# Optimization experiments

Measured on AMD Instinct MI355X. Metric: run time of the kernel, lower is better.

The kernel has to match this reference:

```python
import jax, jax.numpy as jnp
import numpy as np

# --- dims (match init_kwargs) ---
VOCAB = 16; D_MODEL = 512; NLAYERS = 4; LMAX = 1024; NCLASSES = 2
D_STATE = 128; D_CONV = 4; EXPAND = 2; HEADDIM = 64; PAD_IDX = 4
D_INNER = EXPAND * D_MODEL            # 1024
NHEADS = D_INNER // HEADDIM           # 16
CONV_DIM = D_INNER + 2 * D_STATE      # 1280 (ngroups=1)
D_IN_PROJ = 2 * D_INNER + 2 * D_STATE + NHEADS  # 2320
BATCH = 8; SEQ = 1024
EPS = 1e-5


def silu(x):
    return x * jax.nn.sigmoid(x)


def setup_inputs() -> dict:
    key = jax.random.key(0)
    ks = jax.random.split(key, 24)
    s = 0.02
    emb = jax.random.normal(ks[0], (VOCAB, D_MODEL), jnp.float32) * s
    emb = emb.at[PAD_IDX].set(0.0)  # padding_idx row is zero
    inp = {
        "tokens": jax.random.randint(ks[1], (BATCH, SEQ), 0, VOCAB),
        "attention_mask": jnp.ones((BATCH, SEQ), jnp.float32),
        "emb": emb,
        "pos_emb": jax.random.normal(ks[2], (1, LMAX, D_MODEL), jnp.float32) * s,
        "inp_w": jax.random.normal(ks[3], (D_MODEL, D_MODEL), jnp.float32) * s,
        "inp_b": jnp.zeros((D_MODEL,), jnp.float32),
        "ln_g": jnp.ones((D_MODEL,), jnp.float32),
        "ln_b": jnp.zeros((D_MODEL,), jnp.float32),
        # stacked per-layer Mamba2 params
        "in_proj_w": jax.random.normal(ks[4], (NLAYERS, D_IN_PROJ, D_MODEL), jnp.float32) * s,
        "conv_w": jax.random.normal(ks[5], (NLAYERS, CONV_DIM, D_CONV), jnp.float32) * 0.2,
        "conv_b": jnp.zeros((NLAYERS, CONV_DIM), jnp.float32),
        "dt_bias": jax.random.uniform(ks[6], (NLAYERS, NHEADS), jnp.float32, -4.0, -1.0),
        "A_log": jnp.log(jax.random.uniform(ks[7], (NLAYERS, NHEADS), jnp.float32, 1.0, 16.0)),
        "Dparam": jnp.ones((NLAYERS, NHEADS), jnp.float32),
        "norm_w": jnp.ones((NLAYERS, D_INNER), jnp.float32),
        "out_proj_w": jax.random.normal(ks[8], (NLAYERS, D_MODEL, D_INNER), jnp.float32) * s,
        "pooler_w": jax.random.normal(ks[9], (D_MODEL, D_MODEL), jnp.float32) * s,
        "pooler_b": jnp.zeros((D_MODEL,), jnp.float32),
        "cls_w1": jax.random.normal(ks[10], (D_MODEL // 2, D_MODEL), jnp.float32) * s,
        "cls_b1": jnp.zeros((D_MODEL // 2,), jnp.float32),
        "cls_w2": jax.random.normal(ks[11], (NCLASSES, D_MODEL // 2), jnp.float32) * s,
        "cls_b2": jnp.zeros((NCLASSES,), jnp.float32),
    }
    return inp


def mamba2_block(x, in_proj_w, conv_w, conv_b, dt_bias, A_log, Dp, norm_w, out_proj_w):
    """Mamba2 (ngroups=1, no proj biases, conv bias) on x:(B,L,d_model)."""
    Bsz, L, _ = x.shape
    zxbcdt = jnp.einsum("bld,ed->ble", x, in_proj_w)  # (B,L,2320)
    z = zxbcdt[..., :D_INNER]
    xBC = zxbcdt[..., D_INNER:D_INNER + CONV_DIM]
    dt = zxbcdt[..., D_INNER + CONV_DIM:]             # (B,L,H)
    # causal depthwise conv1d + silu
    xp = jnp.pad(xBC, ((0, 0), (D_CONV - 1, 0), (0, 0)))
    conv = conv_b
    for k in range(D_CONV):
        conv = conv + xp[:, k:k + L, :] * conv_w[:, k]
    xBC = silu(conv)
    xh = xBC[..., :D_INNER].reshape(Bsz, L, NHEADS, HEADDIM)
    Bc = xBC[..., D_INNER:D_INNER + D_STATE]          # (B,L,N)
    Cc = xBC[..., D_INNER + D_STATE:]                 # (B,L,N)
    dt = jax.nn.softplus(dt + dt_bias)                # (B,L,H)
    A = -jnp.exp(A_log)                               # (H,)
    dA = jnp.exp(dt * A)                              # (B,L,H)

    def step(h, inp):
        x_t, B_t, C_t, dt_t, dA_t = inp  # (B,H,P),(B,N),(B,N),(B,H),(B,H)
        h = h * dA_t[:, :, None, None] + (dt_t[:, :, None] * x_t)[..., None] * B_t[:, None, None, :]
        y = jnp.einsum("bhpn,bn->bhp", h, C_t)
        return h, y

    h0 = jnp.zeros((Bsz, NHEADS, HEADDIM, D_STATE), x.dtype)
    xs = (xh.transpose(1, 0, 2, 3), Bc.transpose(1, 0, 2), Cc.transpose(1, 0, 2),
          dt.transpose(1, 0, 2), dA.transpose(1, 0, 2))
    _, ys = jax.lax.scan(step, h0, xs)                # (L,B,H,P)
    y = ys.transpose(1, 0, 2, 3) + Dp[None, None, :, None] * xh
    y = y.reshape(Bsz, L, D_INNER)
    # gated RMSNorm: rmsnorm(y * silu(z)) * weight
    y = y * silu(z)
    y = y * jax.lax.rsqrt(jnp.mean(y * y, axis=-1, keepdims=True) + EPS) * norm_w
    return jnp.einsum("ble,de->bld", y, out_proj_w)


def reference(tokens, attention_mask, emb, pos_emb, inp_w, inp_b, ln_g, ln_b,
              in_proj_w, conv_w, conv_b, dt_bias, A_log, Dparam, norm_w, out_proj_w,
              pooler_w, pooler_b, cls_w1, cls_b1, cls_w2, cls_b2):
    L = tokens.shape[1]
    x = emb[tokens] + pos_emb[:, :L, :]
    # input_block: Linear -> LayerNorm (dropout is identity at eval)
    x = jnp.einsum("bld,ed->ble", x, inp_w) + inp_b
    mu = jnp.mean(x, -1, keepdims=True)
    var = jnp.mean((x - mu) ** 2, -1, keepdims=True)
    x = (x - mu) * jax.lax.rsqrt(var + EPS) * ln_g + ln_b
    x = x * attention_mask[..., None]
    for i in range(NLAYERS):
        res = x
        x = mamba2_block(x, in_proj_w[i], conv_w[i], conv_b[i], dt_bias[i],
                         A_log[i], Dparam[i], norm_w[i], out_proj_w[i])
        x = res + x
        x = x * attention_mask[..., None]
    pooled = (jnp.mean(x, axis=1) + jnp.max(x, axis=1)) * 0.5
    pooled = jax.nn.gelu(jnp.einsum("bd,ed->be", pooled, pooler_w) + pooler_b)
    h = jax.nn.gelu(jnp.einsum("bd,ed->be", pooled, cls_w1) + cls_b1)
    return jnp.einsum("bd,ed->be", h, cls_w2) + cls_b2
```

## Files before the change

### kernel.cpp

```cpp
#include <hip/hip_runtime.h>

#define EPS 1e-5f
typedef unsigned short u16;
typedef short s16x8 __attribute__((ext_vector_type(8)));
typedef float f32x4 __attribute__((ext_vector_type(4)));

__device__ __forceinline__ float siluf(float x) { return x / (1.0f + __expf(-x)); }
__device__ __forceinline__ float geluf(float x) {
    float u = 0.7978845608028654f * (x + 0.044715f * x * x * x);
    return 0.5f * x * (1.0f + tanhf(u));
}
__device__ __forceinline__ u16 f2bf(float f) {
    unsigned u = __float_as_uint(f);
    return (u16)((u + 0x7fffu + ((u >> 16) & 1u)) >> 16);
}
__device__ __forceinline__ float bf2f(u16 v) {
    return __uint_as_float(((unsigned)v) << 16);
}
struct u16x4 { u16 x, y, z, w; };
__device__ __forceinline__ u16x4 f2bf4(float4 v) {
    u16x4 r; r.x = f2bf(v.x); r.y = f2bf(v.y); r.z = f2bf(v.z); r.w = f2bf(v.w);
    return r;
}

#define GLOAD_LDS16(gp, lp) __builtin_amdgcn_global_load_lds( \
    (const __attribute__((address_space(1))) void*)(gp),      \
    (__attribute__((address_space(3))) void*)(lp), 16, 0, 0)

__global__ void k_casts(const float* __restrict__ ip, const float* __restrict__ op,
                        const float* __restrict__ inp, u16* __restrict__ wip,
                        u16* __restrict__ wop, u16* __restrict__ winp) {
    int idx = blockIdx.x * 256 + threadIdx.x;
    if (idx < 1245184) {
        int e4 = idx * 4;
        int layer = e4 / 1245184;
        int rem   = e4 - layer * 1245184;
        int row   = rem >> 9;
        int k     = rem & 511;
        float4 v = make_float4(0.f, 0.f, 0.f, 0.f);
        if (row < 2320)
            v = *(const float4*)(ip + (size_t)layer * 1187840 + (size_t)row * 512 + k);
        *(u16x4*)(wip + e4) = f2bf4(v);
    } else if (idx < 1245184 + 524288) {
        int j = idx - 1245184;
        float4 v = *(const float4*)(op + (size_t)j * 4);
        *(u16x4*)(wop + (size_t)j * 4) = f2bf4(v);
    } else if (idx < 1245184 + 524288 + 65536) {
        int j = idx - 1245184 - 524288;
        float4 v = *(const float4*)(inp + (size_t)j * 4);
        *(u16x4*)(winp + (size_t)j * 4) = f2bf4(v);
    }
}

__global__ void k_embed(const int* __restrict__ tok, const float* __restrict__ emb,
                        const float* __restrict__ pos, u16* __restrict__ out) {
    int idx = blockIdx.x * 256 + threadIdx.x;
    int d4 = idx & 127;
    int bl = idx >> 7;
    int l  = bl & 1023;
    float4 e = *(const float4*)(emb + tok[bl] * 512 + d4 * 4);
    float4 p = *(const float4*)(pos + l * 512 + d4 * 4);
    float4 v = make_float4(e.x + p.x, e.y + p.y, e.z + p.z, e.w + p.w);
    *(u16x4*)(out + (size_t)idx * 4) = f2bf4(v);
}

#define STAGE_I(buf, k0) do {                                                   \
    _Pragma("unroll")                                                           \
    for (int s_ = 0; s_ < 2; s_++) {                                            \
        int g_ = w * 2 + s_;                                                    \
        GLOAD_LDS16(A + (size_t)(m0 + g_ * 16 + lr) * 512 + (k0) + lk,          \
                    &Asm[buf][g_ * 512]);                                       \
    }                                                                           \
    GLOAD_LDS16(B + (size_t)(n0 + w * 16 + lr) * 512 + (k0) + lk,               \
                &Bsm[buf][w * 512]);                                            \
    } while (0)

#define COMPUTE_I(buf) do {                                                     \
    s16x8 af_[4], bf_[4];                                                       \
    _Pragma("unroll")                                                           \
    for (int i_ = 0; i_ < 4; i_++) {                                            \
        af_[i_] = *(const s16x8*)&Asm[buf][(wr * 4 + i_) * 512 + l * 8];        \
        bf_[i_] = *(const s16x8*)&Bsm[buf][(wc * 4 + i_) * 512 + l * 8];        \
    }                                                                           \
    _Pragma("unroll")                                                           \
    for (int i_ = 0; i_ < 4; i_++)                                              \
        _Pragma("unroll")                                                       \
        for (int j_ = 0; j_ < 4; j_++)                                          \
            acc[i_][j_] = __builtin_amdgcn_mfma_f32_16x16x32_bf16(              \
                af_[i_], bf_[j_], acc[i_][j_], 0, 0, 0);                        \
    } while (0)

__global__ __launch_bounds__(512, 4) void k_gemm_in(
    const u16* __restrict__ A, const u16* __restrict__ B,
    u16* __restrict__ zbf, u16* __restrict__ xbcbf, float* __restrict__ dtw) {
    __shared__ u16 Asm[3][8192];
    __shared__ u16 Bsm[3][4096];
    const int t = threadIdx.x;
    const int w = t >> 6, l = t & 63;
    const int wr = w >> 1, wc = w & 1;
    const int lr = l & 15, lk = (l >> 4) * 8;
    const int wgid = (blockIdx.x & 7) * 76 + (blockIdx.x >> 3);
    const int m0 = (wgid / 19) * 256;
    const int n0 = (wgid % 19) * 128;

    f32x4 acc[4][4] = {};

    STAGE_I(0, 0);
    STAGE_I(1, 32);
    for (int ki = 0; ki < 14; ki++) {
        asm volatile("s_waitcnt vmcnt(3)" ::: "memory");
        __builtin_amdgcn_s_barrier();
        STAGE_I((ki + 2) % 3, (ki + 2) * 32);
        COMPUTE_I(ki % 3);
    }
    asm volatile("s_waitcnt vmcnt(3)" ::: "memory");
    __builtin_amdgcn_s_barrier();
    COMPUTE_I(14 % 3);
    asm volatile("s_waitcnt vmcnt(0)" ::: "memory");
    __builtin_amdgcn_s_barrier();
    COMPUTE_I(15 % 3);

#pragma unroll
    for (int i = 0; i < 4; i++) {
        int mb = m0 + wr * 64 + i * 16 + (l >> 4) * 4;
#pragma unroll
        for (int j = 0; j < 4; j++) {
            int n = n0 + wc * 64 + j * 16 + (l & 15);
#pragma unroll
            for (int r2 = 0; r2 < 4; r2++) {
                int m = mb + r2;
                float v = acc[i][j][r2];
                if (n < 1024)      zbf[(size_t)m * 1024 + n] = f2bf(v);
                else if (n < 2304) xbcbf[(size_t)m * 1280 + (n - 1024)] = f2bf(v);
                else if (n < 2320) dtw[(size_t)m * 16 + (n - 2304)] = v;
            }
        }
    }
}

#define STAGE(buf, k0) do {                                                     \
    GLOAD_LDS16(A + (size_t)(m0 + w * 16 + lr) * K + (k0) + lk,                 \
                &Asm[buf][w * 512]);                                            \
    GLOAD_LDS16(B + (size_t)(n0 + w * 16 + lr) * K + (k0) + lk,                 \
                &Bsm[buf][w * 512]);                                            \
    } while (0)

#define COMPUTE(buf) do {                                                       \
    s16x8 af_[4], bf_[2];                                                       \
    _Pragma("unroll")                                                           \
    for (int i_ = 0; i_ < 4; i_++)                                              \
        af_[i_] = *(const s16x8*)&Asm[buf][(wr * 4 + i_) * 512 + l * 8];        \
    _Pragma("unroll")                                                           \
    for (int j_ = 0; j_ < 2; j_++)                                              \
        bf_[j_] = *(const s16x8*)&Bsm[buf][(wc * 2 + j_) * 512 + l * 8];        \
    _Pragma("unroll")                                                           \
    for (int i_ = 0; i_ < 4; i_++)                                              \
        _Pragma("unroll")                                                       \
        for (int j_ = 0; j_ < 2; j_++)                                          \
            acc[i_][j_] = __builtin_amdgcn_mfma_f32_16x16x32_bf16(              \
                af_[i_], bf_[j_], acc[i_][j_], 0, 0, 0);                        \
    } while (0)

template <int MODE>
__global__ __launch_bounds__(512) void k_gemm_mfma(
    const u16* __restrict__ A, const u16* __restrict__ B,
    const float* __restrict__ bias, float* __restrict__ C,
    u16* __restrict__ Cbf, const float* __restrict__ mask,
    int M, int N, int K, int gx) {
    __shared__ u16 Asm[3][4096];
    __shared__ u16 Bsm[3][4096];
    const int t = threadIdx.x;
    const int w = t >> 6, l = t & 63;
    const int wr = w >> 2, wc = w & 3;
    const int lr = l & 15, lk = (l >> 4) * 8;
    const int nwg = gridDim.x;
    const int q = nwg >> 3, r = nwg & 7;
    const int x8 = blockIdx.x & 7, d8 = blockIdx.x >> 3;
    const int wgid = (x8 < r) ? x8 * (q + 1) + d8 : r * (q + 1) + (x8 - r) * q + d8;
    const int m0 = (wgid / gx) * 128;
    const int n0 = (wgid % gx) * 128;

    f32x4 acc[4][2] = {};

    const int nk = K >> 5;
    STAGE(0, 0);
    STAGE(1, 32);
    for (int ki = 0; ki < nk - 2; ki++) {
        asm volatile("s_waitcnt vmcnt(2)" ::: "memory");
        __builtin_amdgcn_s_barrier();
        STAGE((ki + 2) % 3, (ki + 2) * 32);
        COMPUTE(ki % 3);
    }
    asm volatile("s_waitcnt vmcnt(2)" ::: "memory");
    __builtin_amdgcn_s_barrier();
    COMPUTE((nk - 2) % 3);
    asm volatile("s_waitcnt vmcnt(0)" ::: "memory");
    __builtin_amdgcn_s_barrier();
    COMPUTE((nk - 1) % 3);

#pragma unroll
    for (int i = 0; i < 4; i++) {
        int mb = m0 + wr * 64 + i * 16 + (l >> 4) * 4;
#pragma unroll
        for (int j = 0; j < 2; j++) {
            int n = n0 + wc * 32 + j * 16 + (l & 15);
#pragma unroll
            for (int r2 = 0; r2 < 4; r2++) {
                int m = mb + r2;
                float v = acc[i][j][r2];
                if (n < N) {
                    if (MODE == 1) v += bias[n];
                    size_t o = (size_t)m * N + n;
                    if (MODE == 2) {
                        v = (C[o] + v) * mask[m];
                        Cbf[o] = f2bf(v);
                    }
                    C[o] = v;
                }
            }
        }
    }
}

__global__ __launch_bounds__(128) void k_layernorm(
    float* __restrict__ x, const float* __restrict__ g,
    const float* __restrict__ b, const float* __restrict__ mask,
    u16* __restrict__ xbf) {
    __shared__ float2 sbuf[2];
    int bl = blockIdx.x;
    int t  = threadIdx.x;
    float4 v = *(float4*)(x + (size_t)bl * 512 + t * 4);
    float s = v.x + v.y + v.z + v.w;
    float q = v.x * v.x + v.y * v.y + v.z * v.z + v.w * v.w;
    for (int off = 32; off; off >>= 1) {
        s += __shfl_xor(s, off, 64);
        q += __shfl_xor(q, off, 64);
    }
    int wid = t >> 6, lane = t & 63;
    if (lane == 0) sbuf[wid] = make_float2(s, q);
    __syncthreads();
    float ts = sbuf[0].x + sbuf[1].x;
    float tq = sbuf[0].y + sbuf[1].y;
    float mu  = ts * (1.f / 512.f);
    float var = tq * (1.f / 512.f) - mu * mu;
    float inv = 1.0f / sqrtf(var + EPS);
    float mk  = mask[bl];
    float4 gg = *(const float4*)(g + t * 4);
    float4 bb = *(const float4*)(b + t * 4);
    float4 o;
    o.x = ((v.x - mu) * inv * gg.x + bb.x) * mk;
    o.y = ((v.y - mu) * inv * gg.y + bb.y) * mk;
    o.z = ((v.z - mu) * inv * gg.z + bb.z) * mk;
    o.w = ((v.w - mu) * inv * gg.w + bb.w) * mk;
    *(float4*)(x + (size_t)bl * 512 + t * 4) = o;
    *(u16x4*)(xbf + (size_t)bl * 512 + t * 4) = f2bf4(o);
}

__global__ __launch_bounds__(320) void k_conv(
    const u16* __restrict__ xbc_in, const float* __restrict__ cw,
    const float* __restrict__ cb, u16* __restrict__ xhbf,
    u16* __restrict__ bcbf) {
    int bid = blockIdx.x;
    int bl = (bid & 7) * 1024 + (bid >> 3);
    int l  = bl & 1023;
    int c  = threadIdx.x * 4;
    float4 w0 = *(const float4*)(cw + (c + 0) * 4);
    float4 w1 = *(const float4*)(cw + (c + 1) * 4);
    float4 w2 = *(const float4*)(cw + (c + 2) * 4);
    float4 w3 = *(const float4*)(cw + (c + 3) * 4);
    float4 a  = *(const float4*)(cb + c);
#pragma unroll
    for (int k = 0; k < 4; k++) {
        if (l + k - 3 >= 0) {
            u16x4 v = *(const u16x4*)(xbc_in + (size_t)(bl + k - 3) * 1280 + c);
            const float* wk0 = (const float*)&w0;
            const float* wk1 = (const float*)&w1;
            const float* wk2 = (const float*)&w2;
            const float* wk3 = (const float*)&w3;
            a.x = fmaf(bf2f(v.x), wk0[k], a.x);
            a.y = fmaf(bf2f(v.y), wk1[k], a.y);
            a.z = fmaf(bf2f(v.z), wk2[k], a.z);
            a.w = fmaf(bf2f(v.w), wk3[k], a.w);
        }
    }
    float4 o = make_float4(siluf(a.x), siluf(a.y), siluf(a.z), siluf(a.w));
    if (c < 1024)
        *(u16x4*)(xhbf + (size_t)bl * 1024 + c) = f2bf4(o);
    else
        *(u16x4*)(bcbf + (size_t)bl * 256 + (c - 1024)) = f2bf4(o);
}

__global__ __launch_bounds__(256) void k_ssd(
    const u16* __restrict__ xhbf, const u16* __restrict__ bcbf,
    const float* __restrict__ dt_raw, const float* __restrict__ dtbias,
    const float* __restrict__ alog, float* __restrict__ elbuf,
    u16* __restrict__ y16, u16* __restrict__ scb16) {
    int bid = blockIdx.x;
    int bhc = (bid & 7) * 128 + (bid >> 3);
    int c = bhc & 7, h = (bhc >> 3) & 15, b = bhc >> 7;
    const size_t row0 = (size_t)b * 1024 + c * 128;
    const int t = threadIdx.x, w = t >> 6, l = t & 63;
    const int wr = w >> 1, wc = w & 1;
    const int lr = l & 15, lk8 = (l >> 4) * 8;

    __shared__ float cl[128], dtl[128], wv[128];
    __shared__ float csh;
    __shared__ __align__(16) u16 shA[8704];
    __shared__ __align__(16) u16 shB[17408];

    float A = -__expf(alog[h]);
    float v = 0.f;
    if (t < 128) {
        float raw = dt_raw[(row0 + t) * 16 + h] + dtbias[h];
        float s = (raw > 20.f) ? raw : log1pf(__expf(raw));
        dtl[t] = s;
        v = s * A;
        int lane = t & 63;
#pragma unroll
        for (int off = 1; off < 64; off <<= 1) {
            float o = __shfl_up(v, off, 64);
            if (lane >= off) v += o;
        }
        if (t == 63) csh = v;
    }
    __syncthreads();
    if (t >= 64 && t < 128) v += csh;
    if (t < 128) {
        cl[t] = v;
        elbuf[(size_t)bhc * 128 + t] = __expf(v);
    }
    __syncthreads();
    if (t < 128) wv[t] = __expf(cl[127] - cl[t]);

    f32x4 acc[4][4] = {};
    for (int ks = 0; ks < 4; ks++) {
        int k0 = ks * 32;
#pragma unroll
        for (int s = 0; s < 2; s++) {
            int g = w * 2 + s;
            GLOAD_LDS16(bcbf + (row0 + g * 16 + lr) * 256 + 128 + k0 + lk8, &shA[g * 512]);
            GLOAD_LDS16(bcbf + (row0 + g * 16 + lr) * 256 +       k0 + lk8, &shA[4096 + g * 512]);
        }
        __syncthreads();
        s16x8 af[4], bfr[4];
#pragma unroll
        for (int i = 0; i < 4; i++) {
            af[i]  = *(const s16x8*)&shA[(wr * 4 + i) * 512 + l * 8];
            bfr[i] = *(const s16x8*)&shA[4096 + (wc * 4 + i) * 512 + l * 8];
        }
#pragma unroll
        for (int i = 0; i < 4; i++)
#pragma unroll
            for (int j = 0; j < 4; j++)
                acc[i][j] = __builtin_amdgcn_mfma_f32_16x16x32_bf16(af[i], bfr[j], acc[i][j], 0, 0, 0);
        __syncthreads();
    }

#pragma unroll
    for (int jj = 0; jj < 32; jj++) {
        int j = jj * 4 + w;
        float xv = bf2f(xhbf[(row0 + j) * 1024 + h * 64 + l]);
        shA[l * 136 + j] = f2bf(dtl[j] * xv);
    }
    __syncthreads();

    f32x4 acc2[4][2] = {};
    for (int half = 0; half < 2; half++) {
        if (wc == half) {
#pragma unroll
            for (int i = 0; i < 4; i++) {
#pragma unroll
                for (int j = 0; j < 4; j++) {
                    int col = half * 64 + j * 16 + (l & 15);
#pragma unroll
                    for (int r = 0; r < 4; r++) {
                        int row = wr * 64 + i * 16 + (l >> 4) * 4 + r;
                        float e = __expf(fminf(cl[row] - cl[col], 0.f));
                        float pv = (col <= row) ? acc[i][j][r] * e : 0.f;
                        shB[row * 72 + j * 16 + (l & 15)] = f2bf(pv);
                    }
                }
            }
        }
        __syncthreads();
#pragma unroll
        for (int ks = 0; ks < 2; ks++) {
            int kof = ks * 32;
            s16x8 pa[4], ub[2];
#pragma unroll
            for (int i = 0; i < 4; i++)
                pa[i] = *(const s16x8*)&shB[(wr * 64 + i * 16 + lr) * 72 + kof + lk8];
#pragma unroll
            for (int jj = 0; jj < 2; jj++)
                ub[jj] = *(const s16x8*)&shA[(wc * 32 + jj * 16 + lr) * 136 + half * 64 + kof + lk8];
#pragma unroll
            for (int i = 0; i < 4; i++)
#pragma unroll
                for (int jj = 0; jj < 2; jj++)
                    acc2[i][jj] = __builtin_amdgcn_mfma_f32_16x16x32_bf16(pa[i], ub[jj], acc2[i][jj], 0, 0, 0);
        }
        __syncthreads();
    }
#pragma unroll
    for (int i = 0; i < 4; i++)
#pragma unroll
        for (int jj = 0; jj < 2; jj++) {
            int p = wc * 32 + jj * 16 + (l & 15);
#pragma unroll
            for (int r = 0; r < 4; r++) {
                int row = wr * 64 + i * 16 + (l >> 4) * 4 + r;
                y16[(row0 + row) * 1024 + h * 64 + p] = f2bf(acc2[i][jj][r]);
            }
        }

#pragma unroll
    for (int s = 0; s < 64; s++) {
        int j = s * 2 + (w & 1);
        int n = (w >> 1) * 64 + l;
        float bvv = bf2f(bcbf[(row0 + j) * 256 + n]);
        shB[n * 136 + j] = f2bf(wv[j] * bvv);
    }
    __syncthreads();

    f32x4 acc3[4][2] = {};
#pragma unroll
    for (int ks = 0; ks < 4; ks++) {
        int kof = ks * 32;
        s16x8 ua[4], bb[2];
#pragma unroll
        for (int i = 0; i < 4; i++)
            ua[i] = *(const s16x8*)&shA[(i * 16 + lr) * 136 + kof + lk8];
#pragma unroll
        for (int jj = 0; jj < 2; jj++)
            bb[jj] = *(const s16x8*)&shB[(w * 32 + jj * 16 + lr) * 136 + kof + lk8];
#pragma unroll
        for (int i = 0; i < 4; i++)
#pragma unroll
            for (int jj = 0; jj < 2; jj++)
                acc3[i][jj] = __builtin_amdgcn_mfma_f32_16x16x32_bf16(ua[i], bb[jj], acc3[i][jj], 0, 0, 0);
    }
#pragma unroll
    for (int i = 0; i < 4; i++)
#pragma unroll
        for (int jj = 0; jj < 2; jj++) {
            int n = w * 32 + jj * 16 + (l & 15);
#pragma unroll
            for (int r = 0; r < 4; r++) {
                int p = i * 16 + (l >> 4) * 4 + r;
                scb16[(size_t)bhc * 8192 + (size_t)p * 128 + n] = f2bf(acc3[i][jj][r]);
            }
        }
}

__global__ __launch_bounds__(512) void k_states(u16* __restrict__ scb16,
                                                const float* __restrict__ elbuf) {
    int bh = blockIdx.x;
    int t = threadIdx.x;
    float hreg[16];
#pragma unroll
    for (int j = 0; j < 16; j++) hreg[j] = 0.f;
    size_t o = (size_t)t * 16;
    for (int c = 0; c < 8; c++) {
        int bhc = bh * 8 + c;
        float Tc = elbuf[(size_t)bhc * 128 + 127];
        u16* p = scb16 + (size_t)bhc * 8192 + o;
        s16x8 v0 = *(s16x8*)(p);
        s16x8 v1 = *(s16x8*)(p + 8);
        s16x8 o0, o1;
#pragma unroll
        for (int j = 0; j < 8; j++) {
            o0[j] = (short)f2bf(hreg[j]);
            o1[j] = (short)f2bf(hreg[8 + j]);
        }
        *(s16x8*)(p)     = o0;
        *(s16x8*)(p + 8) = o1;
#pragma unroll
        for (int j = 0; j < 8; j++) {
            hreg[j]     = fmaf(Tc, hreg[j],     bf2f((u16)v0[j]));
            hreg[8 + j] = fmaf(Tc, hreg[8 + j], bf2f((u16)v1[j]));
        }
    }
}

__global__ __launch_bounds__(256) void k_inter(
    const u16* __restrict__ xhbf, const u16* __restrict__ bcbf,
    const float* __restrict__ elbuf, const u16* __restrict__ scb16,
    const float* __restrict__ Dp, u16* __restrict__ y16) {
    int bid = blockIdx.x;
    int bhc = (bid & 7) * 128 + (bid >> 3);
    int c = bhc & 7, h = (bhc >> 3) & 15, b = bhc >> 7;
    const size_t row0 = (size_t)b * 1024 + c * 128;
    const int t = threadIdx.x, w = t >> 6, l = t & 63;
    const int wr = w >> 1, wc = w & 1;
    const int lr = l & 15, lk8 = (l >> 4) * 8;
    __shared__ __align__(16) u16 CStg[4096];
    __shared__ __align__(16) u16 HStg[2048];
    __shared__ float el[128];
    if (t < 128) el[t] = elbuf[(size_t)bhc * 128 + t];
    float Dv = Dp[h];

    f32x4 acc[4][2] = {};
    for (int ks = 0; ks < 4; ks++) {
        int k0 = ks * 32;
#pragma unroll
        for (int s = 0; s < 2; s++) {
            int g = w * 2 + s;
            GLOAD_LDS16(bcbf + (row0 + g * 16 + lr) * 256 + 128 + k0 + lk8, &CStg[g * 512]);
        }
        GLOAD_LDS16(scb16 + (size_t)bhc * 8192 + (size_t)(w * 16 + lr) * 128 + k0 + lk8,
                    &HStg[w * 512]);
        __syncthreads();
        s16x8 ca[4], hb[2];
#pragma unroll
        for (int i = 0; i < 4; i++)
            ca[i] = *(const s16x8*)&CStg[(wr * 4 + i) * 512 + l * 8];
#pragma unroll
        for (int jj = 0; jj < 2; jj++)
            hb[jj] = *(const s16x8*)&HStg[(wc * 2 + jj) * 512 + l * 8];
#pragma unroll
        for (int i = 0; i < 4; i++)
#pragma unroll
            for (int jj = 0; jj < 2; jj++)
                acc[i][jj] = __builtin_amdgcn_mfma_f32_16x16x32_bf16(ca[i], hb[jj], acc[i][jj], 0, 0, 0);
        __syncthreads();
    }
#pragma unroll
    for (int i = 0; i < 4; i++)
#pragma unroll
        for (int jj = 0; jj < 2; jj++) {
            int p = wc * 32 + jj * 16 + (l & 15);
#pragma unroll
            for (int r = 0; r < 4; r++) {
                int lrow = wr * 64 + i * 16 + (l >> 4) * 4 + r;
                size_t yo = (row0 + lrow) * 1024 + h * 64 + p;
                float yv = bf2f(y16[yo]) + el[lrow] * acc[i][jj][r]
                         + Dv * bf2f(xhbf[(row0 + lrow) * 1024 + h * 64 + p]);
                y16[yo] = f2bf(yv);
            }
        }
}

__global__ __launch_bounds__(256) void k_gate(
    const u16* __restrict__ y16, const u16* __restrict__ zbf,
    const float* __restrict__ nw, u16* __restrict__ ybf) {
    __shared__ float sbuf[4];
    int bl = blockIdx.x;
    int t  = threadIdx.x;
    u16x4 yv4 = *(const u16x4*)(y16 + (size_t)bl * 1024 + t * 4);
    u16x4 zv4 = *(const u16x4*)(zbf + (size_t)bl * 1024 + t * 4);
    float4 gv;
    gv.x = bf2f(yv4.x) * siluf(bf2f(zv4.x));
    gv.y = bf2f(yv4.y) * siluf(bf2f(zv4.y));
    gv.z = bf2f(yv4.z) * siluf(bf2f(zv4.z));
    gv.w = bf2f(yv4.w) * siluf(bf2f(zv4.w));
    float q = gv.x * gv.x + gv.y * gv.y + gv.z * gv.z + gv.w * gv.w;
    for (int off = 32; off; off >>= 1) q += __shfl_xor(q, off, 64);
    int wid = t >> 6, lane = t & 63;
    if (lane == 0) sbuf[wid] = q;
    __syncthreads();
    float tot = sbuf[0] + sbuf[1] + sbuf[2] + sbuf[3];
    float scale = 1.0f / sqrtf(tot * (1.f / 1024.f) + EPS);
    float4 nv = *(const float4*)(nw + t * 4);
    float4 o;
    o.x = gv.x * scale * nv.x;
    o.y = gv.y * scale * nv.y;
    o.z = gv.z * scale * nv.z;
    o.w = gv.w * scale * nv.w;
    *(u16x4*)(ybf + (size_t)bl * 1024 + t * 4) = f2bf4(o);
}

__global__ __launch_bounds__(256) void k_pool1(const float* __restrict__ x,
                                               float* __restrict__ psum,
                                               float* __restrict__ pmax) {
    int blk = blockIdx.x;
    int b = blk >> 6, lc = blk & 63;
    int t = threadIdx.x;
    const float* px = x + (size_t)b * 524288 + (size_t)lc * 16 * 512;
    float s0 = 0.f, s1 = 0.f, m0 = -3.0e38f, m1 = -3.0e38f;
#pragma unroll
    for (int r = 0; r < 16; r++) {
        float v0 = px[r * 512 + t];
        float v1 = px[r * 512 + t + 256];
        s0 += v0; s1 += v1;
        m0 = fmaxf(m0, v0); m1 = fmaxf(m1, v1);
    }
    psum[(size_t)blk * 512 + t]       = s0;
    psum[(size_t)blk * 512 + t + 256] = s1;
    pmax[(size_t)blk * 512 + t]       = m0;
    pmax[(size_t)blk * 512 + t + 256] = m1;
}

__global__ __launch_bounds__(256) void k_pool2(const float* __restrict__ psum,
                                               const float* __restrict__ pmax,
                                               float* __restrict__ pooled) {
    int idx = blockIdx.x * 256 + threadIdx.x;
    int b = idx >> 9, d = idx & 511;
    float s = 0.f, m = -3.0e38f;
    for (int c = 0; c < 64; c++) {
        s += psum[((size_t)b * 64 + c) * 512 + d];
        m = fmaxf(m, pmax[((size_t)b * 64 + c) * 512 + d]);
    }
    pooled[idx] = 0.5f * (s * (1.f / 1024.f) + m);
}

template <int ACT>
__global__ void k_fc(const float* __restrict__ in, const float* __restrict__ W,
                     const float* __restrict__ bias, float* __restrict__ out,
                     int BN, int N, int K) {
    int idx = blockIdx.x * 64 + threadIdx.x;
    if (idx >= BN) return;
    int b = idx / N, n = idx % N;
    const float* a = in + (size_t)b * K;
    const float* w = W + (size_t)n * K;
    float acc = 0.f;
    for (int k = 0; k < K; k += 4) {
        float4 av = *(const float4*)(a + k);
        float4 wv = *(const float4*)(w + k);
        acc += av.x * wv.x + av.y * wv.y + av.z * wv.z + av.w * wv.w;
    }
    float v = acc + bias[n];
    if (ACT == 1) v = geluf(v);
    out[idx] = v;
}

extern "C" void kernel_launch(void* const* d_in, const int* in_sizes, int n_in,
                              void* d_out, int out_size, void* d_ws, size_t ws_size,
                              hipStream_t stream) {
    (void)in_sizes; (void)n_in; (void)out_size; (void)ws_size;
    const int*   tok        = (const int*)  d_in[0];
    const float* mask       = (const float*)d_in[1];
    const float* emb        = (const float*)d_in[2];
    const float* pos        = (const float*)d_in[3];
    const float* inp_w      = (const float*)d_in[4];
    const float* inp_b      = (const float*)d_in[5];
    const float* ln_g       = (const float*)d_in[6];
    const float* ln_b       = (const float*)d_in[7];
    const float* in_proj_w  = (const float*)d_in[8];
    const float* conv_w     = (const float*)d_in[9];
    const float* conv_b     = (const float*)d_in[10];
    const float* dt_bias    = (const float*)d_in[11];
    const float* A_log      = (const float*)d_in[12];
    const float* Dparam     = (const float*)d_in[13];
    const float* norm_w     = (const float*)d_in[14];
    const float* out_proj_w = (const float*)d_in[15];
    const float* pooler_w   = (const float*)d_in[16];
    const float* pooler_b   = (const float*)d_in[17];
    const float* cls_w1     = (const float*)d_in[18];
    const float* cls_b1     = (const float*)d_in[19];
    const float* cls_w2     = (const float*)d_in[20];
    const float* cls_b2     = (const float*)d_in[21];
    float* out = (float*)d_out;

    float* ws     = (float*)d_ws;
    float* x      = ws;
    float* dt_raw = x + (size_t)8192 * 512;
    float* elbuf  = dt_raw + (size_t)8192 * 16;
    float* psum   = elbuf + 131072;
    float* pmax   = psum + 262144;
    float* pooled = pmax + 262144;
    float* pbuf   = pooled + 4096;
    float* cbuf   = pbuf + 4096;
    u16* x_bf    = (u16*)(cbuf + 2048);
    u16* z_bf    = x_bf + (size_t)8192 * 512;
    u16* xbc_in  = z_bf + (size_t)8192 * 1024;
    u16* y_bf    = xbc_in + (size_t)8192 * 1280;
    u16* xhbf    = y_bf + (size_t)8192 * 1024;
    u16* bcbf    = xhbf + (size_t)8192 * 1024;
    u16* y16     = bcbf + (size_t)8192 * 256;
    u16* wip_bf  = y16 + (size_t)8192 * 1024;
    u16* wop_bf  = wip_bf + (size_t)4 * 2432 * 512;
    u16* winp_bf = wop_bf + (size_t)4 * 512 * 1024;
    u16* xe_bf   = (u16*)y16;
    u16* scb16   = xbc_in;

    k_casts<<<7168, 256, 0, stream>>>(in_proj_w, out_proj_w, inp_w,
                                      wip_bf, wop_bf, winp_bf);

    k_embed<<<4096, 256, 0, stream>>>(tok, emb, pos, xe_bf);
    k_gemm_mfma<1><<<256, 512, 0, stream>>>(xe_bf, winp_bf, inp_b, x, nullptr,
                                            nullptr, 8192, 512, 512, 4);
    k_layernorm<<<8192, 128, 0, stream>>>(x, ln_g, ln_b, mask, x_bf);

    for (int i = 0; i < 4; i++) {
        k_gemm_in<<<608, 512, 0, stream>>>(x_bf, wip_bf + (size_t)i * 2432 * 512,
                                           z_bf, xbc_in, dt_raw);
        k_conv<<<8192, 320, 0, stream>>>(xbc_in, conv_w + (size_t)i * 1280 * 4,
                                         conv_b + (size_t)i * 1280, xhbf, bcbf);
        k_ssd<<<1024, 256, 0, stream>>>(xhbf, bcbf, dt_raw, dt_bias + i * 16,
                                        A_log + i * 16, elbuf, y16, scb16);
        k_states<<<128, 512, 0, stream>>>(scb16, elbuf);
        k_inter<<<1024, 256, 0, stream>>>(xhbf, bcbf, elbuf, scb16,
                                          Dparam + (size_t)i * 16, y16);
        k_gate<<<8192, 256, 0, stream>>>(y16, z_bf, norm_w + (size_t)i * 1024, y_bf);
        k_gemm_mfma<2><<<256, 512, 0, stream>>>(y_bf, wop_bf + (size_t)i * 512 * 1024,
                                                nullptr, x, x_bf, mask,
                                                8192, 512, 1024, 4);
    }

    k_pool1<<<512, 256, 0, stream>>>(x, psum, pmax);
    k_pool2<<<16, 256, 0, stream>>>(psum, pmax, pooled);
    k_fc<1><<<64, 64, 0, stream>>>(pooled, pooler_w, pooler_b, pbuf, 8 * 512, 512, 512);
    k_fc<1><<<32, 64, 0, stream>>>(pbuf, cls_w1, cls_b1, cbuf, 8 * 256, 256, 512);
    k_fc<0><<<1, 64, 0, stream>>>(cbuf, cls_w2, cls_b2, out, 8 * 2, 2, 256);
}
```

Measured before the change: 899.6 us.

## Stage GEMM/SSD epilogues through LDS for vectorized stores and double-buffer SSD loads

The in-projection GEMM epilogue now writes the accumulator tile to shared memory and stores 16-byte rows to the z and xBC outputs, replacing per-element scattered bf16 stores. The SSD intra-chunk and inter-chunk kernels get double-buffered global-to-LDS staging with vmcnt waits, so loads for the next K slice overlap the MFMA work. Their y outputs are also staged through LDS for vectorized read-modify-write. This uses more shared memory and adds barriers, which can lower occupancy.

```diff
diff --git a/kernel.cpp b/kernel.cpp
--- a/kernel.cpp
+++ b/kernel.cpp
@@ -69,18 +69,18 @@
     for (int s_ = 0; s_ < 2; s_++) {                                            \
         int g_ = w * 2 + s_;                                                    \
         GLOAD_LDS16(A + (size_t)(m0 + g_ * 16 + lr) * 512 + (k0) + lk,          \
-                    &Asm[buf][g_ * 512]);                                       \
+                    smem + (buf) * 8192 + g_ * 512);                            \
     }                                                                           \
     GLOAD_LDS16(B + (size_t)(n0 + w * 16 + lr) * 512 + (k0) + lk,               \
-                &Bsm[buf][w * 512]);                                            \
+                smem + 24576 + (buf) * 4096 + w * 512);                         \
     } while (0)
 
 #define COMPUTE_I(buf) do {                                                     \
     s16x8 af_[4], bf_[4];                                                       \
     _Pragma("unroll")                                                           \
     for (int i_ = 0; i_ < 4; i_++) {                                            \
-        af_[i_] = *(const s16x8*)&Asm[buf][(wr * 4 + i_) * 512 + l * 8];        \
-        bf_[i_] = *(const s16x8*)&Bsm[buf][(wc * 4 + i_) * 512 + l * 8];        \
+        af_[i_] = *(const s16x8*)&smem[(buf) * 8192 + (wr * 4 + i_) * 512 + l * 8]; \
+        bf_[i_] = *(const s16x8*)&smem[24576 + (buf) * 4096 + (wc * 4 + i_) * 512 + l * 8]; \
     }                                                                           \
     _Pragma("unroll")                                                           \
     for (int i_ = 0; i_ < 4; i_++)                                              \
@@ -93,15 +93,15 @@
 __global__ __launch_bounds__(512, 4) void k_gemm_in(
     const u16* __restrict__ A, const u16* __restrict__ B,
     u16* __restrict__ zbf, u16* __restrict__ xbcbf, float* __restrict__ dtw) {
-    __shared__ u16 Asm[3][8192];
-    __shared__ u16 Bsm[3][4096];
+    __shared__ __align__(16) u16 smem[36864];
     const int t = threadIdx.x;
     const int w = t >> 6, l = t & 63;
     const int wr = w >> 1, wc = w & 1;
     const int lr = l & 15, lk = (l >> 4) * 8;
     const int wgid = (blockIdx.x & 7) * 76 + (blockIdx.x >> 3);
     const int m0 = (wgid / 19) * 256;
-    const int n0 = (wgid % 19) * 128;
+    const int nt = wgid % 19;
+    const int n0 = nt * 128;
 
     f32x4 acc[4][4] = {};
 
@@ -119,20 +119,50 @@
     asm volatile("s_waitcnt vmcnt(0)" ::: "memory");
     __builtin_amdgcn_s_barrier();
     COMPUTE_I(15 % 3);
-
-#pragma unroll
-    for (int i = 0; i < 4; i++) {
-        int mb = m0 + wr * 64 + i * 16 + (l >> 4) * 4;
-#pragma unroll
-        for (int j = 0; j < 4; j++) {
-            int n = n0 + wc * 64 + j * 16 + (l & 15);
-#pragma unroll
-            for (int r2 = 0; r2 < 4; r2++) {
-                int m = mb + r2;
-                float v = acc[i][j][r2];
-                if (n < 1024)      zbf[(size_t)m * 1024 + n] = f2bf(v);
-                else if (n < 2304) xbcbf[(size_t)m * 1280 + (n - 1024)] = f2bf(v);
-                else if (n < 2320) dtw[(size_t)m * 16 + (n - 2304)] = v;
+    __syncthreads();
+
+    if (nt < 18) {
+#pragma unroll
+        for (int i = 0; i < 4; i++)
+#pragma unroll
+            for (int j = 0; j < 4; j++)
+#pragma unroll
+                for (int r2 = 0; r2 < 4; r2++) {
+                    int erow = wr * 64 + i * 16 + (l >> 4) * 4 + r2;
+                    int ecol = wc * 64 + j * 16 + (l & 15);
+                    smem[erow * 136 + ecol] = f2bf(acc[i][j][r2]);
+                }
+        __syncthreads();
+        if (nt < 8) {
+#pragma unroll
+            for (int it = 0; it < 8; it++) {
+                int v = it * 512 + t;
+                int row = v >> 4, col = (v & 15) * 8;
+                *(s16x8*)&zbf[(size_t)(m0 + row) * 1024 + n0 + col] =
+                    *(const s16x8*)&smem[row * 136 + col];
+            }
+        } else {
+            int nb = n0 - 1024;
+#pragma unroll
+            for (int it = 0; it < 8; it++) {
+                int v = it * 512 + t;
+                int row = v >> 4, col = (v & 15) * 8;
+                *(s16x8*)&xbcbf[(size_t)(m0 + row) * 1280 + nb + col] =
+                    *(const s16x8*)&smem[row * 136 + col];
+            }
+        }
+    } else {
+#pragma unroll
+        for (int i = 0; i < 4; i++) {
+            int mb = m0 + wr * 64 + i * 16 + (l >> 4) * 4;
+#pragma unroll
+            for (int j = 0; j < 4; j++) {
+                int n = n0 + wc * 64 + j * 16 + (l & 15);
+#pragma unroll
+                for (int r2 = 0; r2 < 4; r2++) {
+                    if (n < 2320)
+                        dtw[(size_t)(mb + r2) * 16 + (n - 2304)] = acc[i][j][r2];
+                }
             }
         }
     }
@@ -290,6 +320,16 @@
         *(u16x4*)(bcbf + (size_t)bl * 256 + (c - 1024)) = f2bf4(o);
 }
 
+#define SSD_STAGE(dst, k0) do {                                                 \
+    _Pragma("unroll")                                                           \
+    for (int s_ = 0; s_ < 2; s_++) {                                            \
+        int g_ = w * 2 + s_;                                                    \
+        GLOAD_LDS16(bcbf + (row0 + g_ * 16 + lr) * 256 + 128 + (k0) + lk8,      \
+                    (dst) + g_ * 512);                                          \
+        GLOAD_LDS16(bcbf + (row0 + g_ * 16 + lr) * 256 + (k0) + lk8,            \
+                    (dst) + 4096 + g_ * 512);                                   \
+    } } while (0)
+
 __global__ __launch_bounds__(256) void k_ssd(
     const u16* __restrict__ xhbf, const u16* __restrict__ bcbf,
     const float* __restrict__ dt_raw, const float* __restrict__ dtbias,
@@ -308,10 +348,15 @@
     __shared__ __align__(16) u16 shA[8704];
     __shared__ __align__(16) u16 shB[17408];
 
+    float dtb_h = dtbias[h];
     float A = -__expf(alog[h]);
+    float raw = 0.f;
+    if (t < 128) raw = dt_raw[(row0 + t) * 16 + h] + dtb_h;
+    SSD_STAGE(shA, 0);
+    SSD_STAGE(shB, 32);
+
     float v = 0.f;
     if (t < 128) {
-        float raw = dt_raw[(row0 + t) * 16 + h] + dtbias[h];
         float s = (raw > 20.f) ? raw : log1pf(__expf(raw));
         dtl[t] = s;
         v = s * A;
@@ -334,26 +379,23 @@
 
     f32x4 acc[4][4] = {};
     for (int ks = 0; ks < 4; ks++) {
-        int k0 = ks * 32;
-#pragma unroll
-        for (int s = 0; s < 2; s++) {
-            int g = w * 2 + s;
-            GLOAD_LDS16(bcbf + (row0 + g * 16 + lr) * 256 + 128 + k0 + lk8, &shA[g * 512]);
-            GLOAD_LDS16(bcbf + (row0 + g * 16 + lr) * 256 +       k0 + lk8, &shA[4096 + g * 512]);
-        }
-        __syncthreads();
+        u16* cur = (ks & 1) ? shB : shA;
+        if (ks < 3) asm volatile("s_waitcnt vmcnt(4)" ::: "memory");
+        else        asm volatile("s_waitcnt vmcnt(0)" ::: "memory");
+        __builtin_amdgcn_s_barrier();
         s16x8 af[4], bfr[4];
 #pragma unroll
         for (int i = 0; i < 4; i++) {
-            af[i]  = *(const s16x8*)&shA[(wr * 4 + i) * 512 + l * 8];
-            bfr[i] = *(const s16x8*)&shA[4096 + (wc * 4 + i) * 512 + l * 8];
+            af[i]  = *(const s16x8*)&cur[(wr * 4 + i) * 512 + l * 8];
+            bfr[i] = *(const s16x8*)&cur[4096 + (wc * 4 + i) * 512 + l * 8];
         }
 #pragma unroll
         for (int i = 0; i < 4; i++)
 #pragma unroll
             for (int j = 0; j < 4; j++)
                 acc[i][j] = __builtin_amdgcn_mfma_f32_16x16x32_bf16(af[i], bfr[j], acc[i][j], 0, 0, 0);
-        __syncthreads();
+        __builtin_amdgcn_s_barrier();
+        if (ks + 2 < 4) SSD_STAGE(cur, (ks + 2) * 32);
     }
 
 #pragma unroll
@@ -401,17 +443,34 @@
         }
         __syncthreads();
     }
-#pragma unroll
-    for (int i = 0; i < 4; i++)
-#pragma unroll
-        for (int jj = 0; jj < 2; jj++) {
-            int p = wc * 32 + jj * 16 + (l & 15);
-#pragma unroll
-            for (int r = 0; r < 4; r++) {
-                int row = wr * 64 + i * 16 + (l >> 4) * 4 + r;
-                y16[(row0 + row) * 1024 + h * 64 + p] = f2bf(acc2[i][jj][r]);
-            }
-        }
+
+    {
+        float* fb = (float*)shB;
+#pragma unroll
+        for (int i = 0; i < 4; i++)
+#pragma unroll
+            for (int jj = 0; jj < 2; jj++)
+#pragma unroll
+                for (int r = 0; r < 4; r++) {
+                    int row = wr * 64 + i * 16 + (l >> 4) * 4 + r;
+                    fb[row * 68 + wc * 32 + jj * 16 + (l & 15)] = acc2[i][jj][r];
+                }
+        __syncthreads();
+#pragma unroll
+        for (int it = 0; it < 4; it++) {
+            int vv = it * 256 + t;
+            int row = vv >> 3, col = (vv & 7) * 8;
+            float4 f0 = *(const float4*)&fb[row * 68 + col];
+            float4 f1 = *(const float4*)&fb[row * 68 + col + 4];
+            s16x8 ov;
+            const float* p0 = (const float*)&f0;
+            const float* p1 = (const float*)&f1;
+#pragma unroll
+            for (int j = 0; j < 4; j++) { ov[j] = (short)f2bf(p0[j]); ov[4 + j] = (short)f2bf(p1[j]); }
+            *(s16x8*)&y16[(row0 + row) * 1024 + h * 64 + col] = ov;
+        }
+        __syncthreads();
+    }
 
 #pragma unroll
     for (int s = 0; s < 64; s++) {
@@ -481,6 +540,17 @@
         }
     }
 }
+
+#define INT_STAGE(bf_, k0_) do {                                                \
+    _Pragma("unroll")                                                           \
+    for (int s_ = 0; s_ < 2; s_++) {                                            \
+        int g_ = w * 2 + s_;                                                    \
+        GLOAD_LDS16(bcbf + (row0 + g_ * 16 + lr) * 256 + 128 + (k0_) + lk8,     \
+                    &CStg[bf_][g_ * 512]);                                      \
+    }                                                                           \
+    GLOAD_LDS16(scb16 + (size_t)bhc * 8192 + (size_t)(w * 16 + lr) * 128 + (k0_) + lk8, \
+                &HStg[bf_][w * 512]);                                           \
+    } while (0)
 
 __global__ __launch_bounds__(256) void k_inter(
     const u16* __restrict__ xhbf, const u16* __restrict__ bcbf,
@@ -493,51 +563,74 @@
     const int t = threadIdx.x, w = t >> 6, l = t & 63;
     const int wr = w >> 1, wc = w & 1;
     const int lr = l & 15, lk8 = (l >> 4) * 8;
-    __shared__ __align__(16) u16 CStg[4096];
-    __shared__ __align__(16) u16 HStg[2048];
+    __shared__ __align__(16) u16 CStg[2][4096];
+    __shared__ __align__(16) u16 HStg[2][2048];
+    __shared__ __align__(16) float FY[64 * 68];
     __shared__ float el[128];
-    if (t < 128) el[t] = elbuf[(size_t)bhc * 128 + t];
     float Dv = Dp[h];
+    float elv = (t < 128) ? elbuf[(size_t)bhc * 128 + t] : 0.f;
+
+    INT_STAGE(0, 0);
+    INT_STAGE(1, 32);
+    if (t < 128) el[t] = elv;
 
     f32x4 acc[4][2] = {};
     for (int ks = 0; ks < 4; ks++) {
-        int k0 = ks * 32;
-#pragma unroll
-        for (int s = 0; s < 2; s++) {
-            int g = w * 2 + s;
-            GLOAD_LDS16(bcbf + (row0 + g * 16 + lr) * 256 + 128 + k0 + lk8, &CStg[g * 512]);
-        }
-        GLOAD_LDS16(scb16 + (size_t)bhc * 8192 + (size_t)(w * 16 + lr) * 128 + k0 + lk8,
-                    &HStg[w * 512]);
-        __syncthreads();
+        int cur = ks & 1;
+        if (ks < 3) asm volatile("s_waitcnt vmcnt(3)" ::: "memory");
+        else        asm volatile("s_waitcnt vmcnt(0)" ::: "memory");
+        __builtin_amdgcn_s_barrier();
         s16x8 ca[4], hb[2];
 #pragma unroll
         for (int i = 0; i < 4; i++)
-            ca[i] = *(const s16x8*)&CStg[(wr * 4 + i) * 512 + l * 8];
+            ca[i] = *(const s16x8*)&CStg[cur][(wr * 4 + i) * 512 + l * 8];
 #pragma unroll
         for (int jj = 0; jj < 2; jj++)
-            hb[jj] = *(const s16x8*)&HStg[(wc * 2 + jj) * 512 + l * 8];
+            hb[jj] = *(const s16x8*)&HStg[cur][(wc * 2 + jj) * 512 + l * 8];
 #pragma unroll
         for (int i = 0; i < 4; i++)
 #pragma unroll
             for (int jj = 0; jj < 2; jj++)
                 acc[i][jj] = __builtin_amdgcn_mfma_f32_16x16x32_bf16(ca[i], hb[jj], acc[i][jj], 0, 0, 0);
+        __builtin_amdgcn_s_barrier();
+        if (ks + 2 < 4) INT_STAGE(cur, (ks + 2) * 32);
+    }
+
+    for (int ch = 0; ch < 2; ch++) {
+        if (wr == ch) {
+#pragma unroll
+            for (int i = 0; i < 4; i++)
+#pragma unroll
+                for (int jj = 0; jj < 2; jj++)
+#pragma unroll
+                    for (int r = 0; r < 4; r++) {
+                        int rrow = i * 16 + (l >> 4) * 4 + r;
+                        FY[rrow * 68 + wc * 32 + jj * 16 + (l & 15)] =
+                            el[ch * 64 + rrow] * acc[i][jj][r];
+                    }
+        }
         __syncthreads();
-    }
-#pragma unroll
-    for (int i = 0; i < 4; i++)
-#pragma unroll
-        for (int jj = 0; jj < 2; jj++) {
-            int p = wc * 32 + jj * 16 + (l & 15);
-#pragma unroll
-            for (int r = 0; r < 4; r++) {
-                int lrow = wr * 64 + i * 16 + (l >> 4) * 4 + r;
-                size_t yo = (row0 + lrow) * 1024 + h * 64 + p;
-                float yv = bf2f(y16[yo]) + el[lrow] * acc[i][jj][r]
-                         + Dv * bf2f(xhbf[(row0 + lrow) * 1024 + h * 64 + p]);
-                y16[yo] = f2bf(yv);
+#pragma unroll
+        for (int it = 0; it < 2; it++) {
+            int vv = it * 256 + t;
+            int row = vv >> 3, col = (vv & 7) * 8;
+            float4 f0 = *(const float4*)&FY[row * 68 + col];
+            float4 f1 = *(const float4*)&FY[row * 68 + col + 4];
+            size_t yo = (row0 + ch * 64 + row) * 1024 + h * 64 + col;
+            s16x8 yv = *(const s16x8*)&y16[yo];
+            s16x8 xv = *(const s16x8*)&xhbf[yo];
+            s16x8 ov;
+            const float* p0 = (const float*)&f0;
+            const float* p1 = (const float*)&f1;
+#pragma unroll
+            for (int j = 0; j < 4; j++) {
+                ov[j]     = (short)f2bf(bf2f((u16)yv[j])     + p0[j] + Dv * bf2f((u16)xv[j]));
+                ov[4 + j] = (short)f2bf(bf2f((u16)yv[4 + j]) + p1[j] + Dv * bf2f((u16)xv[4 + j]));
             }
-        }
+            *(s16x8*)&y16[yo] = ov;
+        }
+        __syncthreads();
+    }
 }
 
 __global__ __launch_bounds__(256) void k_gate(
```

Result: faster. 834.8 us (-7.2%).
